# Optimization experiments

Measured on AMD Instinct MI355X. Metric: run time of the kernel, lower is better.

The kernel has to match this reference:

```python
import jax, jax.numpy as jnp
import numpy as np

N_TOKENS = 8192   # batch*seq
D_IN = 4096
D_OUT = 4096
RANK = 64


def setup_inputs() -> dict:
    key = jax.random.key(0)
    k_x, k_s, k_u, k_d, k_q = jax.random.split(key, 5)
    x = jax.random.normal(k_x, (N_TOKENS, D_IN), dtype=jnp.float32)
    scales = jax.random.uniform(k_s, (D_OUT, 1), dtype=jnp.float32)
    U = jax.random.normal(k_u, (D_OUT, RANK), dtype=jnp.float32)
    D = jax.random.normal(k_d, (RANK, D_IN), dtype=jnp.float32)
    Q = jax.random.randint(k_q, (D_OUT, D_IN), 0, 127, dtype=jnp.int32)
    return {"x": x, "scales": scales, "U": U, "D": D, "Q": Q}


def reference(x, scales, U, D, Q):
    # Dequantize: Wdq[o, i] = Q[o, i] * scales[o]  -> fp32 [D_OUT, D_IN]
    Wdq = Q.astype(jnp.float32) * scales
    # Main GEMM: [N, D_IN] @ [D_IN, D_OUT]
    main = x @ Wdq.T
    # Low-rank adapter: x @ D.T -> [N, RANK], then @ U.T -> [N, D_OUT]
    adapt = (x @ D.T) @ U.T
    return main + adapt
```

## Files before the change

kernel.cpp:

```cpp
#include <hip/hip_runtime.h>
#include <hip/hip_fp16.h>
#include <cstdint>

#define M_TOK 8192
#define K_IN  4096
#define N_OUT 4096
#define RANK  64
#define KSPLIT 8
#define LDA_P 4160
#define NT_P  65

typedef _Float16 f16x8 __attribute__((ext_vector_type(8)));
typedef _Float16 f16x4 __attribute__((ext_vector_type(4)));
typedef float    f32x4 __attribute__((ext_vector_type(4)));

__device__ __forceinline__ void gld_lds16(const void* g, void* l) {
    __builtin_amdgcn_global_load_lds(
        (const __attribute__((address_space(1))) void*)g,
        (__attribute__((address_space(3))) void*)l,
        16, 0, 0);
}

__global__ void k_cvt_f32_f16(const float4* __restrict__ in,
                              f16x4* __restrict__ out, int n4) {
    int i = blockIdx.x * 256 + threadIdx.x;
    if (i >= n4) return;
    float4 v = in[i];
    f16x4 r;
    r[0] = (_Float16)v.x; r[1] = (_Float16)v.y;
    r[2] = (_Float16)v.z; r[3] = (_Float16)v.w;
    out[i] = r;
}

__global__ void k_cvt_w8(const int4* __restrict__ Q, const float* __restrict__ s,
                         _Float16* __restrict__ WU) {
    int i = blockIdx.x * 256 + threadIdx.x;
    float sc = s[i >> 9];
    int4 q0 = Q[2 * i], q1 = Q[2 * i + 1];
    f16x8 r;
    r[0] = (_Float16)(q0.x * sc); r[1] = (_Float16)(q0.y * sc);
    r[2] = (_Float16)(q0.z * sc); r[3] = (_Float16)(q0.w * sc);
    r[4] = (_Float16)(q1.x * sc); r[5] = (_Float16)(q1.y * sc);
    r[6] = (_Float16)(q1.z * sc); r[7] = (_Float16)(q1.w * sc);
    *(f16x8*)(WU + (size_t)(i >> 9) * LDA_P + (size_t)(i & 511) * 8) = r;
}

__global__ void k_cvt_u(const float* __restrict__ U, _Float16* __restrict__ WU) {
    int i = blockIdx.x * 256 + threadIdx.x;
    int o = i >> 3, c = (i & 7) * 8;
    const float4* up = (const float4*)(U + (size_t)o * RANK + c);
    float4 v0 = up[0], v1 = up[1];
    f16x8 r;
    r[0] = (_Float16)v0.x; r[1] = (_Float16)v0.y;
    r[2] = (_Float16)v0.z; r[3] = (_Float16)v0.w;
    r[4] = (_Float16)v1.x; r[5] = (_Float16)v1.y;
    r[6] = (_Float16)v1.z; r[7] = (_Float16)v1.w;
    *(f16x8*)(WU + (size_t)o * LDA_P + 4096 + c) = r;
}

__global__ __launch_bounds__(256)
void k_t_fused(const float* __restrict__ X, const _Float16* __restrict__ Dh,
               _Float16* __restrict__ XT, float* __restrict__ T32) {
    __shared__ _Float16 Xs[64 * 32];
    __shared__ _Float16 Ds[64 * 32];
    const int tid = threadIdx.x, wave = tid >> 6, lane = tid & 63;
    const int row0 = blockIdx.x * 64;
    const int kbase = blockIdx.y * (K_IN / KSPLIT);
    const int lr = tid >> 2, lk = (tid & 3) * 8;
    const int rr = lane >> 2, c8 = (lane & 3) * 8;
    const int fm = lane & 15, fk = (lane >> 4) * 8;
    f32x4 acc[4] = {};

    for (int kk = 0; kk < K_IN / KSPLIT; kk += 32) {
        const int k0 = kbase + kk;
        const float* gx = X + (size_t)(row0 + lr) * K_IN + k0 + lk;
        float4 v0 = *(const float4*)gx;
        float4 v1 = *(const float4*)(gx + 4);
        f16x8 h;
        h[0] = (_Float16)v0.x; h[1] = (_Float16)v0.y;
        h[2] = (_Float16)v0.z; h[3] = (_Float16)v0.w;
        h[4] = (_Float16)v1.x; h[5] = (_Float16)v1.y;
        h[6] = (_Float16)v1.z; h[7] = (_Float16)v1.w;
        *(f16x8*)(XT + (size_t)(row0 + lr) * LDA_P + k0 + lk) = h;
        *(f16x8*)&Xs[lr * 32 + lk] = h;
        gld_lds16(Dh + (size_t)(wave * 16 + rr) * K_IN + k0 + c8,
                  Ds + wave * 16 * 32);
        __syncthreads();
        f16x8 a = *(const f16x8*)&Xs[(wave * 16 + fm) * 32 + fk];
#pragma unroll
        for (int n = 0; n < 4; n++) {
            f16x8 b = *(const f16x8*)&Ds[(n * 16 + fm) * 32 + fk];
            acc[n] = __builtin_amdgcn_mfma_f32_16x16x32_f16(a, b, acc[n], 0, 0, 0);
        }
        __syncthreads();
    }
#pragma unroll
    for (int n = 0; n < 4; n++)
#pragma unroll
        for (int r = 0; r < 4; r++) {
            int row = row0 + wave * 16 + (lane >> 4) * 4 + r;
            int col = n * 16 + (lane & 15);
            T32[((size_t)blockIdx.y * M_TOK + row) * RANK + col] = acc[n][r];
        }
}

__global__ void k_reduce_t(const float* __restrict__ T32,
                           _Float16* __restrict__ XT) {
    int i = blockIdx.x * 256 + threadIdx.x;
    float s = 0.f;
#pragma unroll
    for (int c = 0; c < KSPLIT; c++)
        s += T32[(size_t)c * M_TOK * RANK + i];
    XT[(size_t)(i >> 6) * LDA_P + 4096 + (i & 63)] = (_Float16)s;
}

__global__ __launch_bounds__(512, 2)
void k_main(const _Float16* __restrict__ XT, const _Float16* __restrict__ WU,
            float* __restrict__ C) {
    __shared__ _Float16 lds[2][2][256 * 64];
    const int tid = threadIdx.x;
    const int wave = tid >> 6, lane = tid & 63;
    const int wr = wave >> 2, wc = wave & 3;
    const int fm = lane & 15, g = lane >> 4;

    int bs = (blockIdx.x & 7) * 64 + (blockIdx.x >> 3);
    const int bx = bs & 15, by = bs >> 4;
    const int arow0 = by * 256, brow0 = bx * 256;

    const int srow = wave * 8 + (lane >> 3);
    const int scol = ((lane & 7) ^ (lane >> 3)) * 8;

    const int ax0 = (g ^ (fm & 7)) * 8;
    const int ax1 = ((4 + g) ^ (fm & 7)) * 8;
    const int aRB = (wr * 128 + fm) * 64;
    const int bRB = (wc * 64 + fm) * 64;

    f32x4 acc[8][4] = {};

    auto stA = [&](int q, int r, int t) {
        gld_lds16(XT + (size_t)(arow0 + r * 64 + srow) * LDA_P + t * 64 + scol,
                  &lds[q][0][(r * 512 + wave * 64) * 8]);
    };
    auto stB = [&](int q, int r, int t) {
        gld_lds16(WU + (size_t)(brow0 + r * 64 + srow) * LDA_P + t * 64 + scol,
                  &lds[q][1][(r * 512 + wave * 64) * 8]);
    };

#define VMC(n) asm volatile("s_waitcnt vmcnt(" #n ")" ::: "memory")
#define PHASE(P, MH, KS, STG, VM) do {                                        \
    const _Float16* Ab = &lds[P][0][0];                                       \
    const _Float16* Bb = &lds[P][1][0];                                       \
    const int ax = (KS ? ax1 : ax0);                                          \
    f16x8 a[4], b[4];                                                         \
    _Pragma("unroll")                                                         \
    for (int m = 0; m < 4; ++m)                                               \
        a[m] = *(const f16x8*)&Ab[aRB + MH * 4096 + m * 1024 + ax];           \
    _Pragma("unroll")                                                         \
    for (int n = 0; n < 4; ++n)                                               \
        b[n] = *(const f16x8*)&Bb[bRB + n * 1024 + ax];                       \
    STG                                                                       \
    __builtin_amdgcn_s_barrier();                                             \
    asm volatile("s_waitcnt lgkmcnt(0)" ::: "memory");                        \
    __builtin_amdgcn_s_setprio(1);                                            \
    _Pragma("unroll")                                                         \
    for (int m = 0; m < 4; ++m)                                               \
        _Pragma("unroll")                                                     \
        for (int n = 0; n < 4; ++n)                                           \
            acc[MH * 4 + m][n] = __builtin_amdgcn_mfma_f32_16x16x32_f16(      \
                a[m], b[n], acc[MH * 4 + m][n], 0, 0, 0);                     \
    __builtin_amdgcn_s_setprio(0);                                            \
    VM;                                                                       \
    __builtin_amdgcn_s_barrier();                                             \
} while (0)

#define TILE(P, T1, T2)                                                       \
    PHASE(P, 0, 0,                                                            \
          { stB(P ^ 1, 0, T1); stB(P ^ 1, 1, T1);                             \
            stB(P ^ 1, 2, T1); stB(P ^ 1, 3, T1); }, );                       \
    PHASE(P, 0, 1, { stA(P ^ 1, 1, T1); stA(P ^ 1, 3, T1); }, VMC(8));        \
    PHASE(P, 1, 0, {;}, );                                                    \
    PHASE(P, 1, 1, { stA(P, 0, T2); stA(P, 2, T2); }, VMC(4))

    stA(0, 0, 0); stA(0, 2, 0);
    stB(0, 0, 0); stB(0, 1, 0); stB(0, 2, 0); stB(0, 3, 0);
    stA(0, 1, 0); stA(0, 3, 0);
    stA(1, 0, 1); stA(1, 2, 1);
    VMC(4);
    __builtin_amdgcn_s_barrier();

#pragma unroll 1
    for (int t = 0; t < NT_P - 1; t += 2) {
        int t2b = t + 3;
        if (t2b >= NT_P) t2b = 0;
        TILE(0, t + 1, t + 2);
        TILE(1, t + 2, t2b);
    }
    TILE(0, 0, 1);

#undef TILE
#undef PHASE
#undef VMC

#pragma unroll
    for (int mi = 0; mi < 8; ++mi) {
        const int row = arow0 + wr * 128 + mi * 16 + g * 4;
#pragma unroll
        for (int n = 0; n < 4; ++n) {
            const int col = brow0 + wc * 64 + n * 16 + fm;
            float* cp = C + (size_t)row * N_OUT + col;
#pragma unroll
            for (int r = 0; r < 4; ++r)
                cp[(size_t)r * N_OUT] = acc[mi][n][r];
        }
    }
}

__global__ void fb_t(const float* __restrict__ x, const float* __restrict__ Dm,
                     float* __restrict__ t) {
    int n = blockIdx.x, r = threadIdx.x;
    const float* xr = x + (size_t)n * K_IN;
    const float* dr = Dm + (size_t)r * K_IN;
    float s = 0.f;
    for (int k = 0; k < K_IN; k++) s += xr[k] * dr[k];
    t[n * RANK + r] = s;
}

__global__ void fb_main(const float* __restrict__ x, const float* __restrict__ scales,
                        const float* __restrict__ U, const int* __restrict__ Q,
                        const float* __restrict__ t, float* __restrict__ out) {
    size_t i = (size_t)blockIdx.x * 256 + threadIdx.x;
    int n = (int)(i >> 12), o = (int)(i & 4095);
    const float* xr = x + (size_t)n * K_IN;
    const int* qr = Q + (size_t)o * K_IN;
    float s = 0.f;
    for (int k = 0; k < K_IN; k++) s += xr[k] * (float)qr[k];
    float a = 0.f;
    const float* tr = t + (size_t)n * RANK;
    const float* ur = U + (size_t)o * RANK;
    for (int r = 0; r < RANK; r++) a += tr[r] * ur[r];
    out[i] = scales[o] * s + a;
}

extern "C" void kernel_launch(void* const* d_in, const int* in_sizes, int n_in,
                              void* d_out, int out_size, void* d_ws, size_t ws_size,
                              hipStream_t stream) {
    const float* x      = (const float*)d_in[0];
    const float* scales = (const float*)d_in[1];
    const float* U      = (const float*)d_in[2];
    const float* D      = (const float*)d_in[3];
    const int*   Q      = (const int*)d_in[4];
    float* out = (float*)d_out;

    const size_t SZ_XT  = (size_t)M_TOK * LDA_P * 2;
    const size_t SZ_WU  = (size_t)N_OUT * LDA_P * 2;
    const size_t SZ_D   = (size_t)RANK * K_IN * 2;
    const size_t SZ_T32 = (size_t)KSPLIT * M_TOK * RANK * 4;
    const size_t NEED   = SZ_XT + SZ_WU + SZ_D + SZ_T32;

    if (ws_size >= NEED) {
        char* w = (char*)d_ws;
        _Float16* XT  = (_Float16*)w; w += SZ_XT;
        _Float16* WU  = (_Float16*)w; w += SZ_WU;
        _Float16* Dh  = (_Float16*)w; w += SZ_D;
        float*    T32 = (float*)w;

        k_cvt_f32_f16<<<256, 256, 0, stream>>>((const float4*)D, (f16x4*)Dh,
                                               RANK * K_IN / 4);
        k_t_fused<<<dim3(M_TOK / 64, KSPLIT), 256, 0, stream>>>(x, Dh, XT, T32);
        k_reduce_t<<<M_TOK * RANK / 256, 256, 0, stream>>>(T32, XT);
        k_cvt_w8<<<N_OUT * K_IN / 8 / 256, 256, 0, stream>>>((const int4*)Q,
                                                             scales, WU);
        k_cvt_u<<<N_OUT * RANK / 8 / 256, 256, 0, stream>>>(U, WU);
        k_main<<<512, 512, 0, stream>>>(XT, WU, out);
    } else {
        float* t32 = (float*)d_ws;
        fb_t<<<M_TOK, RANK, 0, stream>>>(x, D, t32);
        fb_main<<<(int)((size_t)M_TOK * N_OUT / 256), 256, 0, stream>>>(
            x, scales, U, Q, t32, out);
    }
}
```

Measured before the change: 544.6 us.

## Split x conversion from low-rank GEMM and reuse B fragments in main kernel

```diff
diff --git a/kernel.cpp b/kernel.cpp
--- a/kernel.cpp
+++ b/kernel.cpp
@@ -30,6 +30,20 @@
     r[0] = (_Float16)v.x; r[1] = (_Float16)v.y;
     r[2] = (_Float16)v.z; r[3] = (_Float16)v.w;
     out[i] = r;
+}
+
+__global__ __launch_bounds__(256)
+void k_cvt_x(const float4* __restrict__ X, _Float16* __restrict__ XT) {
+    for (int i = blockIdx.x * 256 + threadIdx.x; i < M_TOK * K_IN / 8;
+         i += gridDim.x * 256) {
+        float4 v0 = X[2 * i], v1 = X[2 * i + 1];
+        f16x8 h;
+        h[0] = (_Float16)v0.x; h[1] = (_Float16)v0.y;
+        h[2] = (_Float16)v0.z; h[3] = (_Float16)v0.w;
+        h[4] = (_Float16)v1.x; h[5] = (_Float16)v1.y;
+        h[6] = (_Float16)v1.z; h[7] = (_Float16)v1.w;
+        *(f16x8*)(XT + (size_t)(i >> 9) * LDA_P + (size_t)(i & 511) * 8) = h;
+    }
 }
 
 __global__ void k_cvt_w8(const int4* __restrict__ Q, const float* __restrict__ s,
@@ -59,38 +73,46 @@
 }
 
 __global__ __launch_bounds__(256)
-void k_t_fused(const float* __restrict__ X, const _Float16* __restrict__ Dh,
-               _Float16* __restrict__ XT, float* __restrict__ T32) {
-    __shared__ _Float16 Xs[64 * 32];
-    __shared__ _Float16 Ds[64 * 32];
+void k_t(const _Float16* __restrict__ Xh, const _Float16* __restrict__ Dh,
+         float* __restrict__ T32) {
+    __shared__ _Float16 Xs[2][64 * 64];
+    __shared__ _Float16 Ds[2][64 * 64];
     const int tid = threadIdx.x, wave = tid >> 6, lane = tid & 63;
     const int row0 = blockIdx.x * 64;
     const int kbase = blockIdx.y * (K_IN / KSPLIT);
-    const int lr = tid >> 2, lk = (tid & 3) * 8;
-    const int rr = lane >> 2, c8 = (lane & 3) * 8;
-    const int fm = lane & 15, fk = (lane >> 4) * 8;
+    const int srow8 = lane >> 3;
+    const int scol = ((lane & 7) ^ srow8) * 8;
+    const int fm = lane & 15, g = lane >> 4;
+    const int ax0 = (g ^ (fm & 7)) * 8;
+    const int ax1 = ((4 + g) ^ (fm & 7)) * 8;
     f32x4 acc[4] = {};
 
-    for (int kk = 0; kk < K_IN / KSPLIT; kk += 32) {
-        const int k0 = kbase + kk;
-        const float* gx = X + (size_t)(row0 + lr) * K_IN + k0 + lk;
-        float4 v0 = *(const float4*)gx;
-        float4 v1 = *(const float4*)(gx + 4);
-        f16x8 h;
-        h[0] = (_Float16)v0.x; h[1] = (_Float16)v0.y;
-        h[2] = (_Float16)v0.z; h[3] = (_Float16)v0.w;
-        h[4] = (_Float16)v1.x; h[5] = (_Float16)v1.y;
-        h[6] = (_Float16)v1.z; h[7] = (_Float16)v1.w;
-        *(f16x8*)(XT + (size_t)(row0 + lr) * LDA_P + k0 + lk) = h;
-        *(f16x8*)&Xs[lr * 32 + lk] = h;
-        gld_lds16(Dh + (size_t)(wave * 16 + rr) * K_IN + k0 + c8,
-                  Ds + wave * 16 * 32);
-        __syncthreads();
-        f16x8 a = *(const f16x8*)&Xs[(wave * 16 + fm) * 32 + fk];
-#pragma unroll
-        for (int n = 0; n < 4; n++) {
-            f16x8 b = *(const f16x8*)&Ds[(n * 16 + fm) * 32 + fk];
-            acc[n] = __builtin_amdgcn_mfma_f32_16x16x32_f16(a, b, acc[n], 0, 0, 0);
+    auto stage = [&](int buf, int it) {
+        const int k0 = kbase + it * 64;
+#pragma unroll
+        for (int c = 0; c < 2; ++c) {
+            int slab = wave * 2 + c;
+            gld_lds16(Xh + (size_t)(row0 + slab * 8 + srow8) * LDA_P + k0 + scol,
+                      &Xs[buf][slab * 8 * 64]);
+            gld_lds16(Dh + (size_t)(slab * 8 + srow8) * K_IN + k0 + scol,
+                      &Ds[buf][slab * 8 * 64]);
+        }
+    };
+
+    stage(0, 0);
+    __syncthreads();
+#pragma unroll 1
+    for (int it = 0; it < K_IN / KSPLIT / 64; ++it) {
+        int buf = it & 1;
+        if (it < K_IN / KSPLIT / 64 - 1) stage(buf ^ 1, it + 1);
+        f16x8 a0 = *(const f16x8*)&Xs[buf][(wave * 16 + fm) * 64 + ax0];
+        f16x8 a1 = *(const f16x8*)&Xs[buf][(wave * 16 + fm) * 64 + ax1];
+#pragma unroll
+        for (int n = 0; n < 4; ++n) {
+            f16x8 b0 = *(const f16x8*)&Ds[buf][(n * 16 + fm) * 64 + ax0];
+            acc[n] = __builtin_amdgcn_mfma_f32_16x16x32_f16(a0, b0, acc[n], 0, 0, 0);
+            f16x8 b1 = *(const f16x8*)&Ds[buf][(n * 16 + fm) * 64 + ax1];
+            acc[n] = __builtin_amdgcn_mfma_f32_16x16x32_f16(a1, b1, acc[n], 0, 0, 0);
         }
         __syncthreads();
     }
@@ -98,8 +120,8 @@
     for (int n = 0; n < 4; n++)
 #pragma unroll
         for (int r = 0; r < 4; r++) {
-            int row = row0 + wave * 16 + (lane >> 4) * 4 + r;
-            int col = n * 16 + (lane & 15);
+            int row = row0 + wave * 16 + g * 4 + r;
+            int col = n * 16 + fm;
             T32[((size_t)blockIdx.y * M_TOK + row) * RANK + col] = acc[n][r];
         }
 }
@@ -136,6 +158,7 @@
     const int bRB = (wc * 64 + fm) * 64;
 
     f32x4 acc[8][4] = {};
+    f16x8 b[4];
 
     auto stA = [&](int q, int r, int t) {
         gld_lds16(XT + (size_t)(arow0 + r * 64 + srow) * LDA_P + t * 64 + scol,
@@ -147,17 +170,19 @@
     };
 
 #define VMC(n) asm volatile("s_waitcnt vmcnt(" #n ")" ::: "memory")
-#define PHASE(P, MH, KS, STG, VM) do {                                        \
+#define PHASE(P, MH, KS, RB, STG, VM) do {                                    \
     const _Float16* Ab = &lds[P][0][0];                                       \
     const _Float16* Bb = &lds[P][1][0];                                       \
     const int ax = (KS ? ax1 : ax0);                                          \
-    f16x8 a[4], b[4];                                                         \
+    f16x8 a[4];                                                               \
     _Pragma("unroll")                                                         \
     for (int m = 0; m < 4; ++m)                                               \
         a[m] = *(const f16x8*)&Ab[aRB + MH * 4096 + m * 1024 + ax];           \
-    _Pragma("unroll")                                                         \
-    for (int n = 0; n < 4; ++n)                                               \
-        b[n] = *(const f16x8*)&Bb[bRB + n * 1024 + ax];                       \
+    if (RB) {                                                                 \
+        _Pragma("unroll")                                                     \
+        for (int n = 0; n < 4; ++n)                                           \
+            b[n] = *(const f16x8*)&Bb[bRB + n * 1024 + ax];                   \
+    }                                                                         \
     STG                                                                       \
     __builtin_amdgcn_s_barrier();                                             \
     asm volatile("s_waitcnt lgkmcnt(0)" ::: "memory");                        \
@@ -173,13 +198,13 @@
     __builtin_amdgcn_s_barrier();                                             \
 } while (0)
 
-#define TILE(P, T1, T2)                                                       \
-    PHASE(P, 0, 0,                                                            \
-          { stB(P ^ 1, 0, T1); stB(P ^ 1, 1, T1);                             \
-            stB(P ^ 1, 2, T1); stB(P ^ 1, 3, T1); }, );                       \
-    PHASE(P, 0, 1, { stA(P ^ 1, 1, T1); stA(P ^ 1, 3, T1); }, VMC(8));        \
-    PHASE(P, 1, 0, {;}, );                                                    \
-    PHASE(P, 1, 1, { stA(P, 0, T2); stA(P, 2, T2); }, VMC(4))
+#define TILE(P, TB, TA)                                                       \
+    PHASE(P, 0, 0, 1,                                                         \
+          { stB(P ^ 1, 0, TB); stB(P ^ 1, 1, TB);                             \
+            stB(P ^ 1, 2, TB); stB(P ^ 1, 3, TB); }, VMC(6));                 \
+    PHASE(P, 1, 0, 0, { stA(P ^ 1, 1, TB); stA(P ^ 1, 3, TB); }, );           \
+    PHASE(P, 0, 1, 1, {;}, );                                                 \
+    PHASE(P, 1, 1, 0, { stA(P, 0, TA); stA(P, 2, TA); }, VMC(4))
 
     stA(0, 0, 0); stA(0, 2, 0);
     stB(0, 0, 0); stB(0, 1, 0); stB(0, 2, 0); stB(0, 3, 0);
@@ -190,10 +215,10 @@
 
 #pragma unroll 1
     for (int t = 0; t < NT_P - 1; t += 2) {
-        int t2b = t + 3;
-        if (t2b >= NT_P) t2b = 0;
+        int t3 = t + 3;
+        if (t3 >= NT_P) t3 = 0;
         TILE(0, t + 1, t + 2);
-        TILE(1, t + 2, t2b);
+        TILE(1, t + 2, t3);
     }
     TILE(0, 0, 1);
 
@@ -266,7 +291,8 @@
 
         k_cvt_f32_f16<<<256, 256, 0, stream>>>((const float4*)D, (f16x4*)Dh,
                                                RANK * K_IN / 4);
-        k_t_fused<<<dim3(M_TOK / 64, KSPLIT), 256, 0, stream>>>(x, Dh, XT, T32);
+        k_cvt_x<<<2048, 256, 0, stream>>>((const float4*)x, XT);
+        k_t<<<dim3(M_TOK / 64, KSPLIT), 256, 0, stream>>>(XT, Dh, T32);
         k_reduce_t<<<M_TOK * RANK / 256, 256, 0, stream>>>(T32, XT);
         k_cvt_w8<<<N_OUT * K_IN / 8 / 256, 256, 0, stream>>>((const int4*)Q,
                                                              scales, WU);
```

After: 523.3 us. 1.04x faster.
